# Performance work log

Measured on AMD Instinct MI355X. Metric: run time of the kernel, lower is better.

The kernel has to match this reference:

```python
import jax, jax.numpy as jnp
import numpy as np


def setup_inputs() -> dict:
    key = jax.random.key(0)
    ks = jax.random.split(key, 7)
    LAG, N, NREG, NT, H = 5, 4096, 500, 500, 16
    s = 0.05  # keep activations in a sane range
    return {
        "AX": jax.random.normal(ks[0], (LAG, N, NREG), dtype=jnp.float32),
        "W0": jax.random.normal(ks[1], (H * NT, NREG, LAG), dtype=jnp.float32) * s,
        "b0": jax.random.normal(ks[2], (H * NT,), dtype=jnp.float32) * s,
        "W1": jax.random.normal(ks[3], (NT, H, H), dtype=jnp.float32) * s,
        "b1": jax.random.normal(ks[4], (NT, H), dtype=jnp.float32) * s,
        "W2": jax.random.normal(ks[5], (NT, 1, H), dtype=jnp.float32) * s,
        "b2": jax.random.normal(ks[6], (NT, 1), dtype=jnp.float32) * s,
    }


def reference(AX, W0, b0, W1, b1, W2, b2):
    # First layer: sum_i AX[i] @ W0[:,:,lag-1-i].T + b0, fused over lag.
    # AX: [lag, N, n_regs]; W0: [hidden0*n_targets, n_regs, lag]
    x = jnp.einsum('lnr,orl->no', AX, W0[:, :, ::-1]) + b0  # [N, hidden0*nt]
    N = x.shape[0]
    nt, d1, d0 = W1.shape  # [n_targets, d_out, d_in]
    # Grouped 1x1 convs == independent per-target GEMMs; channels are target-major.
    x = x.reshape(N, nt, d0)
    x = jax.nn.relu(x)
    x = jnp.einsum('ntd,ted->nte', x, W1) + b1  # [N, nt, d1]
    x = jax.nn.relu(x)
    x = jnp.einsum('nte,tfe->ntf', x, W2) + b2  # [N, nt, 1]
    return x[..., 0]  # [N, n_targets]
```

## Files before the change

### kernel.cpp

```cpp
#include <hip/hip_runtime.h>
#include <hip/hip_bf16.h>
#include <stdint.h>

#define LAG 5
#define NROW 4096
#define NREG 500
#define NTGT 500
#define O_REAL 8000
#define KP 2560
#define NPAD 8192
#define BK 64
#define NT 40

typedef __bf16 bf16x8 __attribute__((ext_vector_type(8)));
typedef float f32x4 __attribute__((ext_vector_type(4)));

__device__ __forceinline__ unsigned short f2bf(float f) {
  unsigned u = __float_as_uint(f);
  return (unsigned short)((u + 0x7fffu + ((u >> 16) & 1u)) >> 16);
}

__device__ __forceinline__ void async16(void* lds_base, const void* g) {
  __builtin_amdgcn_global_load_lds(
      (const __attribute__((address_space(1))) unsigned int*)g,
      (__attribute__((address_space(3))) unsigned int*)lds_base,
      16, 0, 0);
}

__global__ __launch_bounds__(256) void convA(const float* __restrict__ AX,
                                             unsigned short* __restrict__ Ab) {
  int idx = blockIdx.x * 256 + threadIdx.x;
  if (idx >= NROW * (KP / 4)) return;
  int n = idx / (KP / 4);
  int c4 = idx - n * (KP / 4);
  int k = c4 * 4;
  ushort4 o;
  if (k < LAG * NREG) {
    int l = k / NREG, r = k - l * NREG;
    float4 v = *(const float4*)(AX + ((size_t)l * NROW + n) * NREG + r);
    o.x = f2bf(v.x); o.y = f2bf(v.y); o.z = f2bf(v.z); o.w = f2bf(v.w);
  } else {
    o.x = 0; o.y = 0; o.z = 0; o.w = 0;
  }
  *(ushort4*)(Ab + (size_t)idx * 4) = o;
}

__global__ __launch_bounds__(256) void convB(const float* __restrict__ W0,
                                             unsigned short* __restrict__ Bb) {
  int idx = blockIdx.x * 256 + threadIdx.x;
  if (idx >= O_REAL * NREG) return;
  int o = idx / NREG, r = idx - o * NREG;
  const float* s = W0 + (size_t)idx * LAG;
  #pragma unroll
  for (int j = 0; j < LAG; ++j)
    Bb[(size_t)o * KP + (size_t)(LAG - 1 - j) * NREG + r] = f2bf(s[j]);
}

__global__ __launch_bounds__(256) void padB(unsigned short* __restrict__ Bb) {
  int idx = blockIdx.x * 256 + threadIdx.x;
  const int A4 = O_REAL * 15;
  ushort4 z; z.x = 0; z.y = 0; z.z = 0; z.w = 0;
  if (idx < A4) {
    int row = idx / 15, c4 = idx - row * 15;
    *(ushort4*)(Bb + (size_t)row * KP + 2500 + c4 * 4) = z;
  } else {
    int j = idx - A4;
    if (j < 192 * (KP / 4))
      *(ushort4*)(Bb + (size_t)O_REAL * KP + (size_t)j * 4) = z;
  }
}

__global__ __launch_bounds__(512, 2) void gemm8(const unsigned short* __restrict__ A,
                                                const unsigned short* __restrict__ B,
                                                const float* __restrict__ b0,
                                                const float* __restrict__ W1g,
                                                const float* __restrict__ b1g,
                                                const float* __restrict__ W2g,
                                                const float* __restrict__ b2g,
                                                float* __restrict__ out) {
  extern __shared__ char smem[];
  char* sAc = smem;
  char* sBc = smem + 65536;

  int bid = blockIdx.x;
  int swz = (bid & 7) * 64 + (bid >> 3);
  int mt = swz & 15, ntile = swz >> 4;
  int row0 = mt * 256, col0 = ntile * 256;

  int tid = threadIdx.x, l = tid & 63, w = tid >> 6;
  int wr = w >> 2, wc = w & 3;

  int sr = l >> 3;
  int ss = (l & 7) ^ sr;
  const unsigned short* gApre0 = A + (size_t)(row0 + (w * 2 + 0) * 8 + sr) * KP + ss * 8;
  const unsigned short* gApre1 = A + (size_t)(row0 + (w * 2 + 1) * 8 + sr) * KP + ss * 8;
  const unsigned short* gBpre0 = B + (size_t)(col0 + (w * 2 + 0) * 8 + sr) * KP + ss * 8;
  const unsigned short* gBpre1 = B + (size_t)(col0 + (w * 2 + 1) * 8 + sr) * KP + ss * 8;

#define STG_A(buf, half, t) do { \
    async16(sAc + (buf) * 32768 + (half) * 16384 + (w * 2 + 0) * 1024, gApre0 + (size_t)(half) * 128 * KP + (size_t)(t) * BK); \
    async16(sAc + (buf) * 32768 + (half) * 16384 + (w * 2 + 1) * 1024, gApre1 + (size_t)(half) * 128 * KP + (size_t)(t) * BK); \
  } while (0)
#define STG_B(buf, half, t) do { \
    async16(sBc + (buf) * 32768 + (half) * 16384 + (w * 2 + 0) * 1024, gBpre0 + (size_t)(half) * 128 * KP + (size_t)(t) * BK); \
    async16(sBc + (buf) * 32768 + (half) * 16384 + (w * 2 + 1) * 1024, gBpre1 + (size_t)(half) * 128 * KP + (size_t)(t) * BK); \
  } while (0)

  int arowb = (wr * 128 + (l & 15)) * 128;
  int browb = (wc * 64 + (l & 15)) * 128;
  int c0 = (((l >> 4) << 4)) ^ ((l & 7) << 4);

  auto lda = [&](int buf, int mi, int kk) -> bf16x8 {
    return *(const bf16x8*)(sAc + buf * 32768 + arowb + mi * 2048 + (c0 ^ (kk * 64)));
  };
  auto ldb = [&](int buf, int ni, int kk) -> bf16x8 {
    return *(const bf16x8*)(sBc + buf * 32768 + browb + ni * 2048 + (c0 ^ (kk * 64)));
  };

  f32x4 acc[8][4];
  #pragma unroll
  for (int i = 0; i < 8; ++i)
    #pragma unroll
    for (int j = 0; j < 4; ++j) acc[i][j] = (f32x4){0.f, 0.f, 0.f, 0.f};

#define PH_SYNC() do { __builtin_amdgcn_s_barrier(); \
    asm volatile("s_waitcnt lgkmcnt(0)" ::: "memory"); \
    __builtin_amdgcn_s_setprio(1); } while (0)
#define PH_END() do { __builtin_amdgcn_s_setprio(0); __builtin_amdgcn_s_barrier(); } while (0)

#define MFMA_Q(MOFF, AF, NIOFF) do { \
    _Pragma("unroll") \
    for (int mi = 0; mi < 4; ++mi) { \
      _Pragma("unroll") \
      for (int ni = 0; ni < 2; ++ni) { \
        acc[(MOFF) + mi][(NIOFF) + ni] = __builtin_amdgcn_mfma_f32_16x16x32_bf16(AF[mi][0], bb[(NIOFF) + ni][0], acc[(MOFF) + mi][(NIOFF) + ni], 0, 0, 0); \
        acc[(MOFF) + mi][(NIOFF) + ni] = __builtin_amdgcn_mfma_f32_16x16x32_bf16(AF[mi][1], bb[(NIOFF) + ni][1], acc[(MOFF) + mi][(NIOFF) + ni], 0, 0, 0); \
      } \
    } \
  } while (0)

  STG_B(0, 0, 0); STG_B(0, 1, 0); STG_A(0, 0, 0); STG_A(0, 1, 0);
  STG_B(1, 0, 1); STG_B(1, 1, 1);
  asm volatile("s_waitcnt vmcnt(4)" ::: "memory");
  __builtin_amdgcn_s_barrier();

  for (int t = 0; t < NT; t += 2) {
    const bool last = (t == NT - 2);
    bf16x8 a03[4][2], a47[4][2], bb[4][2];

    #pragma unroll
    for (int ni = 0; ni < 2; ++ni) { bb[ni][0] = ldb(0, ni, 0); bb[ni][1] = ldb(0, ni, 1); }
    #pragma unroll
    for (int mi = 0; mi < 4; ++mi) { a03[mi][0] = lda(0, mi, 0); a03[mi][1] = lda(0, mi, 1); }
    STG_A(1, 0, t + 1);
    asm volatile("s_waitcnt lgkmcnt(8)" ::: "memory");
    PH_SYNC(); MFMA_Q(0, a03, 0); PH_END();

    #pragma unroll
    for (int ni = 2; ni < 4; ++ni) { bb[ni][0] = ldb(0, ni, 0); bb[ni][1] = ldb(0, ni, 1); }
    STG_A(1, 1, t + 1);
    PH_SYNC(); MFMA_Q(0, a03, 2); PH_END();

    #pragma unroll
    for (int mi = 0; mi < 4; ++mi) { a47[mi][0] = lda(0, 4 + mi, 0); a47[mi][1] = lda(0, 4 + mi, 1); }
    if (!last) STG_B(0, 0, t + 2);
    PH_SYNC(); MFMA_Q(4, a47, 0); PH_END();

    if (!last) STG_B(0, 1, t + 2);
    if (last) asm volatile("s_waitcnt vmcnt(0)" ::: "memory");
    else      asm volatile("s_waitcnt vmcnt(4)" ::: "memory");
    __builtin_amdgcn_s_barrier();
    asm volatile("s_waitcnt lgkmcnt(0)" ::: "memory");
    __builtin_amdgcn_s_setprio(1);
    MFMA_Q(4, a47, 2);
    PH_END();

    #pragma unroll
    for (int ni = 0; ni < 2; ++ni) { bb[ni][0] = ldb(1, ni, 0); bb[ni][1] = ldb(1, ni, 1); }
    #pragma unroll
    for (int mi = 0; mi < 4; ++mi) { a03[mi][0] = lda(1, mi, 0); a03[mi][1] = lda(1, mi, 1); }
    if (!last) STG_A(0, 0, t + 2);
    asm volatile("s_waitcnt lgkmcnt(8)" ::: "memory");
    PH_SYNC(); MFMA_Q(0, a03, 0); PH_END();

    #pragma unroll
    for (int ni = 2; ni < 4; ++ni) { bb[ni][0] = ldb(1, ni, 0); bb[ni][1] = ldb(1, ni, 1); }
    if (!last) STG_A(0, 1, t + 2);
    PH_SYNC(); MFMA_Q(0, a03, 2); PH_END();

    #pragma unroll
    for (int mi = 0; mi < 4; ++mi) { a47[mi][0] = lda(1, 4 + mi, 0); a47[mi][1] = lda(1, 4 + mi, 1); }
    if (!last) STG_B(1, 0, t + 3);
    PH_SYNC(); MFMA_Q(4, a47, 0); PH_END();

    if (!last) STG_B(1, 1, t + 3);
    if (last) asm volatile("s_waitcnt vmcnt(0)" ::: "memory");
    else      asm volatile("s_waitcnt vmcnt(4)" ::: "memory");
    __builtin_amdgcn_s_barrier();
    asm volatile("s_waitcnt lgkmcnt(0)" ::: "memory");
    __builtin_amdgcn_s_setprio(1);
    MFMA_Q(4, a47, 2);
    __builtin_amdgcn_s_setprio(0);
    __builtin_amdgcn_s_barrier();
  }

  int lq = l >> 4, lr = l & 15;
  int t0 = col0 >> 4;

  float bias[4];
  #pragma unroll
  for (int ni = 0; ni < 4; ++ni) {
    int gcol = col0 + wc * 64 + ni * 16 + lr;
    bias[ni] = (gcol < O_REAL) ? b0[gcol] : 0.f;
  }

  #pragma unroll
  for (int mi = 0; mi < 8; ++mi) {
    #pragma unroll
    for (int ni = 0; ni < 4; ++ni) {
      #pragma unroll
      for (int r = 0; r < 4; ++r) {
        int rowL = wr * 128 + mi * 16 + lq * 4 + r;
        int colL = wc * 64 + ni * 16 + lr;
        int sw = ((rowL ^ (rowL >> 2)) & 7) << 4;
        float v = fmaxf(acc[mi][ni][r] + bias[ni], 0.f);
        *(unsigned short*)(smem + (size_t)rowL * 512 + ((colL * 2) ^ sw)) = f2bf(v);
      }
    }
  }
  __syncthreads();

  int uw = __builtin_amdgcn_readfirstlane(w);
  float oacc[2][4];
  #pragma unroll
  for (int g = 0; g < 2; ++g) {
    int tloc = uw * 2 + g;
    int tt = t0 + tloc;
    bool tvalid = (tt < NTGT);
    const float* w1t = W1g + (size_t)tt * 256;
    float b1v[16], w2v[16];
    float b2v = 0.f;
    if (tvalid) {
      #pragma unroll
      for (int e4 = 0; e4 < 4; ++e4) {
        float4 ba = *(const float4*)(b1g + (size_t)tt * 16 + e4 * 4);
        float4 wa = *(const float4*)(W2g + (size_t)tt * 16 + e4 * 4);
        b1v[e4 * 4 + 0] = ba.x; b1v[e4 * 4 + 1] = ba.y; b1v[e4 * 4 + 2] = ba.z; b1v[e4 * 4 + 3] = ba.w;
        w2v[e4 * 4 + 0] = wa.x; w2v[e4 * 4 + 1] = wa.y; w2v[e4 * 4 + 2] = wa.z; w2v[e4 * 4 + 3] = wa.w;
      }
      b2v = b2g[tt];
    }
    #pragma unroll
    for (int rg = 0; rg < 4; ++rg) {
      int rowL = rg * 64 + l;
      int sw = ((rowL ^ (rowL >> 2)) & 7) << 4;
      const char* bp = smem + (size_t)rowL * 512;
      uint4 va = *(const uint4*)(bp + ((tloc * 32) ^ sw));
      uint4 vb = *(const uint4*)(bp + ((tloc * 32 + 16) ^ sw));
      unsigned q0 = va.x, q1 = va.y, q2 = va.z, q3 = va.w;
      unsigned q4 = vb.x, q5 = vb.y, q6 = vb.z, q7 = vb.w;
      float x[16];
      x[0]  = __uint_as_float(q0 << 16); x[1]  = __uint_as_float(q0 & 0xffff0000u);
      x[2]  = __uint_as_float(q1 << 16); x[3]  = __uint_as_float(q1 & 0xffff0000u);
      x[4]  = __uint_as_float(q2 << 16); x[5]  = __uint_as_float(q2 & 0xffff0000u);
      x[6]  = __uint_as_float(q3 << 16); x[7]  = __uint_as_float(q3 & 0xffff0000u);
      x[8]  = __uint_as_float(q4 << 16); x[9]  = __uint_as_float(q4 & 0xffff0000u);
      x[10] = __uint_as_float(q5 << 16); x[11] = __uint_as_float(q5 & 0xffff0000u);
      x[12] = __uint_as_float(q6 << 16); x[13] = __uint_as_float(q6 & 0xffff0000u);
      x[14] = __uint_as_float(q7 << 16); x[15] = __uint_as_float(q7 & 0xffff0000u);
      float o = 0.f;
      if (tvalid) {
        #pragma unroll
        for (int e = 0; e < 16; ++e) {
          float4 wq0 = *(const float4*)(w1t + e * 16 + 0);
          float4 wq1 = *(const float4*)(w1t + e * 16 + 4);
          float4 wq2 = *(const float4*)(w1t + e * 16 + 8);
          float4 wq3 = *(const float4*)(w1t + e * 16 + 12);
          float s = b1v[e];
          s = fmaf(x[0],  wq0.x, s); s = fmaf(x[1],  wq0.y, s);
          s = fmaf(x[2],  wq0.z, s); s = fmaf(x[3],  wq0.w, s);
          s = fmaf(x[4],  wq1.x, s); s = fmaf(x[5],  wq1.y, s);
          s = fmaf(x[6],  wq1.z, s); s = fmaf(x[7],  wq1.w, s);
          s = fmaf(x[8],  wq2.x, s); s = fmaf(x[9],  wq2.y, s);
          s = fmaf(x[10], wq2.z, s); s = fmaf(x[11], wq2.w, s);
          s = fmaf(x[12], wq3.x, s); s = fmaf(x[13], wq3.y, s);
          s = fmaf(x[14], wq3.z, s); s = fmaf(x[15], wq3.w, s);
          s = fmaxf(s, 0.f);
          o = fmaf(s, w2v[e], o);
        }
        o += b2v;
      }
      oacc[g][rg] = o;
    }
  }
  __syncthreads();

  {
    float* sOut = (float*)smem;
    #pragma unroll
    for (int g = 0; g < 2; ++g) {
      int tloc = uw * 2 + g;
      #pragma unroll
      for (int rg = 0; rg < 4; ++rg)
        sOut[(rg * 64 + l) * 17 + tloc] = oacc[g][rg];
    }
    __syncthreads();
    int c = tid & 15, rr = tid >> 4;
    bool cv = (t0 + c < NTGT);
    #pragma unroll
    for (int j = 0; j < 8; ++j) {
      int row = rr + 32 * j;
      if (cv) out[(size_t)(row0 + row) * NTGT + (t0 + c)] = sOut[row * 17 + c];
    }
  }
#undef STG_A
#undef STG_B
#undef PH_SYNC
#undef PH_END
#undef MFMA_Q
}

extern "C" void kernel_launch(void* const* d_in, const int* in_sizes, int n_in,
                              void* d_out, int out_size, void* d_ws, size_t ws_size,
                              hipStream_t stream) {
  const float* AX = (const float*)d_in[0];
  const float* W0 = (const float*)d_in[1];
  const float* b0 = (const float*)d_in[2];
  const float* W1 = (const float*)d_in[3];
  const float* b1 = (const float*)d_in[4];
  const float* W2 = (const float*)d_in[5];
  const float* b2 = (const float*)d_in[6];
  float* out = (float*)d_out;

  char* ws = (char*)d_ws;
  const size_t szA = (size_t)NROW * KP * 2;
  unsigned short* Ab = (unsigned short*)ws;
  unsigned short* Bb = (unsigned short*)(ws + szA);

  hipFuncSetAttribute((const void*)gemm8, hipFuncAttributeMaxDynamicSharedMemorySize, 131072);

  convA<<<(NROW * (KP / 4) + 255) / 256, 256, 0, stream>>>(AX, Ab);
  convB<<<(O_REAL * NREG + 255) / 256, 256, 0, stream>>>(W0, Bb);
  {
    int npad4 = O_REAL * 15 + 192 * (KP / 4);
    padB<<<(npad4 + 255) / 256, 256, 0, stream>>>(Bb);
  }
  gemm8<<<(NROW / 256) * (NPAD / 256), 512, 131072, stream>>>(Ab, Bb, b0, W1, b1, W2, b2, out);
}
```

Baseline: 207.6 us.

## Switch GEMM inner loop from 16x16x32 to 32x32x16 bf16 MFMA tiles

Replaces the 16x16x32 bf16 MFMA tiling with 32x32x16 MFMA instructions. Each wave now holds 4x2 f32x16 accumulators instead of 8x4 f32x4, and the LDS fragment addressing, swizzle and epilogue row/column mapping are rewritten to match the 32x32 output layout. The aim is fewer MFMA issues and fewer LDS fragment reads per K-step, since the larger instruction reuses each operand more. The risk is a different LDS bank-conflict pattern from the new swizzle and higher register pressure from the larger fragment arrays.

```diff
diff --git a/kernel.cpp b/kernel.cpp
--- a/kernel.cpp
+++ b/kernel.cpp
@@ -14,6 +14,7 @@
 
 typedef __bf16 bf16x8 __attribute__((ext_vector_type(8)));
 typedef float f32x4 __attribute__((ext_vector_type(4)));
+typedef float f32x16 __attribute__((ext_vector_type(16)));
 
 __device__ __forceinline__ unsigned short f2bf(float f) {
   unsigned u = __float_as_uint(f);
@@ -106,36 +107,36 @@
     async16(sBc + (buf) * 32768 + (half) * 16384 + (w * 2 + 1) * 1024, gBpre1 + (size_t)(half) * 128 * KP + (size_t)(t) * BK); \
   } while (0)
 
-  int arowb = (wr * 128 + (l & 15)) * 128;
-  int browb = (wc * 64 + (l & 15)) * 128;
-  int c0 = (((l >> 4) << 4)) ^ ((l & 7) << 4);
-
-  auto lda = [&](int buf, int mi, int kk) -> bf16x8 {
-    return *(const bf16x8*)(sAc + buf * 32768 + arowb + mi * 2048 + (c0 ^ (kk * 64)));
+  int hi = l >> 5;
+  int sw8 = (l & 7) << 4;
+  int arowb = (wr * 128 + (l & 31)) * 128;
+  int browb = (wc * 64 + (l & 31)) * 128;
+
+  auto lda32 = [&](int buf, int mi, int ks) -> bf16x8 {
+    return *(const bf16x8*)(sAc + buf * 32768 + arowb + mi * 4096 + ((((ks * 2 + hi) << 4)) ^ sw8));
   };
-  auto ldb = [&](int buf, int ni, int kk) -> bf16x8 {
-    return *(const bf16x8*)(sBc + buf * 32768 + browb + ni * 2048 + (c0 ^ (kk * 64)));
+  auto ldb32 = [&](int buf, int ni, int ks) -> bf16x8 {
+    return *(const bf16x8*)(sBc + buf * 32768 + browb + ni * 4096 + ((((ks * 2 + hi) << 4)) ^ sw8));
   };
 
-  f32x4 acc[8][4];
-  #pragma unroll
-  for (int i = 0; i < 8; ++i)
-    #pragma unroll
-    for (int j = 0; j < 4; ++j) acc[i][j] = (f32x4){0.f, 0.f, 0.f, 0.f};
+  f32x16 acc[4][2];
+  #pragma unroll
+  for (int i = 0; i < 4; ++i)
+    #pragma unroll
+    for (int j = 0; j < 2; ++j)
+      #pragma unroll
+      for (int r = 0; r < 16; ++r) acc[i][j][r] = 0.f;
 
 #define PH_SYNC() do { __builtin_amdgcn_s_barrier(); \
     asm volatile("s_waitcnt lgkmcnt(0)" ::: "memory"); \
     __builtin_amdgcn_s_setprio(1); } while (0)
 #define PH_END() do { __builtin_amdgcn_s_setprio(0); __builtin_amdgcn_s_barrier(); } while (0)
 
-#define MFMA_Q(MOFF, AF, NIOFF) do { \
+#define MFMA_P(M0, AF, BV, NI) do { \
     _Pragma("unroll") \
-    for (int mi = 0; mi < 4; ++mi) { \
-      _Pragma("unroll") \
-      for (int ni = 0; ni < 2; ++ni) { \
-        acc[(MOFF) + mi][(NIOFF) + ni] = __builtin_amdgcn_mfma_f32_16x16x32_bf16(AF[mi][0], bb[(NIOFF) + ni][0], acc[(MOFF) + mi][(NIOFF) + ni], 0, 0, 0); \
-        acc[(MOFF) + mi][(NIOFF) + ni] = __builtin_amdgcn_mfma_f32_16x16x32_bf16(AF[mi][1], bb[(NIOFF) + ni][1], acc[(MOFF) + mi][(NIOFF) + ni], 0, 0, 0); \
-      } \
+    for (int ks = 0; ks < 4; ++ks) { \
+      acc[(M0) + 0][NI] = __builtin_amdgcn_mfma_f32_32x32x16_bf16(AF[0][ks], BV[ks], acc[(M0) + 0][NI], 0, 0, 0); \
+      acc[(M0) + 1][NI] = __builtin_amdgcn_mfma_f32_32x32x16_bf16(AF[1][ks], BV[ks], acc[(M0) + 1][NI], 0, 0, 0); \
     } \
   } while (0)
 
@@ -146,25 +147,29 @@
 
   for (int t = 0; t < NT; t += 2) {
     const bool last = (t == NT - 2);
-    bf16x8 a03[4][2], a47[4][2], bb[4][2];
-
-    #pragma unroll
-    for (int ni = 0; ni < 2; ++ni) { bb[ni][0] = ldb(0, ni, 0); bb[ni][1] = ldb(0, ni, 1); }
-    #pragma unroll
-    for (int mi = 0; mi < 4; ++mi) { a03[mi][0] = lda(0, mi, 0); a03[mi][1] = lda(0, mi, 1); }
+    bf16x8 a01[2][4], a23[2][4], b0v[4], b1v[4];
+
+    #pragma unroll
+    for (int ks = 0; ks < 4; ++ks) b0v[ks] = ldb32(0, 0, ks);
+    #pragma unroll
+    for (int mi = 0; mi < 2; ++mi)
+      #pragma unroll
+      for (int ks = 0; ks < 4; ++ks) a01[mi][ks] = lda32(0, mi, ks);
     STG_A(1, 0, t + 1);
     asm volatile("s_waitcnt lgkmcnt(8)" ::: "memory");
-    PH_SYNC(); MFMA_Q(0, a03, 0); PH_END();
-
-    #pragma unroll
-    for (int ni = 2; ni < 4; ++ni) { bb[ni][0] = ldb(0, ni, 0); bb[ni][1] = ldb(0, ni, 1); }
+    PH_SYNC(); MFMA_P(0, a01, b0v, 0); PH_END();
+
+    #pragma unroll
+    for (int ks = 0; ks < 4; ++ks) b1v[ks] = ldb32(0, 1, ks);
     STG_A(1, 1, t + 1);
-    PH_SYNC(); MFMA_Q(0, a03, 2); PH_END();
-
-    #pragma unroll
-    for (int mi = 0; mi < 4; ++mi) { a47[mi][0] = lda(0, 4 + mi, 0); a47[mi][1] = lda(0, 4 + mi, 1); }
+    PH_SYNC(); MFMA_P(0, a01, b1v, 1); PH_END();
+
+    #pragma unroll
+    for (int mi = 0; mi < 2; ++mi)
+      #pragma unroll
+      for (int ks = 0; ks < 4; ++ks) a23[mi][ks] = lda32(0, 2 + mi, ks);
     if (!last) STG_B(0, 0, t + 2);
-    PH_SYNC(); MFMA_Q(4, a47, 0); PH_END();
+    PH_SYNC(); MFMA_P(2, a23, b0v, 0); PH_END();
 
     if (!last) STG_B(0, 1, t + 2);
     if (last) asm volatile("s_waitcnt vmcnt(0)" ::: "memory");
@@ -172,26 +177,30 @@
     __builtin_amdgcn_s_barrier();
     asm volatile("s_waitcnt lgkmcnt(0)" ::: "memory");
     __builtin_amdgcn_s_setprio(1);
-    MFMA_Q(4, a47, 2);
+    MFMA_P(2, a23, b1v, 1);
     PH_END();
 
     #pragma unroll
-    for (int ni = 0; ni < 2; ++ni) { bb[ni][0] = ldb(1, ni, 0); bb[ni][1] = ldb(1, ni, 1); }
-    #pragma unroll
-    for (int mi = 0; mi < 4; ++mi) { a03[mi][0] = lda(1, mi, 0); a03[mi][1] = lda(1, mi, 1); }
+    for (int ks = 0; ks < 4; ++ks) b0v[ks] = ldb32(1, 0, ks);
+    #pragma unroll
+    for (int mi = 0; mi < 2; ++mi)
+      #pragma unroll
+      for (int ks = 0; ks < 4; ++ks) a01[mi][ks] = lda32(1, mi, ks);
     if (!last) STG_A(0, 0, t + 2);
     asm volatile("s_waitcnt lgkmcnt(8)" ::: "memory");
-    PH_SYNC(); MFMA_Q(0, a03, 0); PH_END();
-
-    #pragma unroll
-    for (int ni = 2; ni < 4; ++ni) { bb[ni][0] = ldb(1, ni, 0); bb[ni][1] = ldb(1, ni, 1); }
+    PH_SYNC(); MFMA_P(0, a01, b0v, 0); PH_END();
+
+    #pragma unroll
+    for (int ks = 0; ks < 4; ++ks) b1v[ks] = ldb32(1, 1, ks);
     if (!last) STG_A(0, 1, t + 2);
-    PH_SYNC(); MFMA_Q(0, a03, 2); PH_END();
-
-    #pragma unroll
-    for (int mi = 0; mi < 4; ++mi) { a47[mi][0] = lda(1, 4 + mi, 0); a47[mi][1] = lda(1, 4 + mi, 1); }
+    PH_SYNC(); MFMA_P(0, a01, b1v, 1); PH_END();
+
+    #pragma unroll
+    for (int mi = 0; mi < 2; ++mi)
+      #pragma unroll
+      for (int ks = 0; ks < 4; ++ks) a23[mi][ks] = lda32(1, 2 + mi, ks);
     if (!last) STG_B(1, 0, t + 3);
-    PH_SYNC(); MFMA_Q(4, a47, 0); PH_END();
+    PH_SYNC(); MFMA_P(2, a23, b0v, 0); PH_END();
 
     if (!last) STG_B(1, 1, t + 3);
     if (last) asm volatile("s_waitcnt vmcnt(0)" ::: "memory");
@@ -199,31 +208,30 @@
     __builtin_amdgcn_s_barrier();
     asm volatile("s_waitcnt lgkmcnt(0)" ::: "memory");
     __builtin_amdgcn_s_setprio(1);
-    MFMA_Q(4, a47, 2);
+    MFMA_P(2, a23, b1v, 1);
     __builtin_amdgcn_s_setprio(0);
     __builtin_amdgcn_s_barrier();
   }
 
-  int lq = l >> 4, lr = l & 15;
   int t0 = col0 >> 4;
 
-  float bias[4];
-  #pragma unroll
-  for (int ni = 0; ni < 4; ++ni) {
-    int gcol = col0 + wc * 64 + ni * 16 + lr;
-    bias[ni] = (gcol < O_REAL) ? b0[gcol] : 0.f;
-  }
-
-  #pragma unroll
-  for (int mi = 0; mi < 8; ++mi) {
-    #pragma unroll
-    for (int ni = 0; ni < 4; ++ni) {
-      #pragma unroll
-      for (int r = 0; r < 4; ++r) {
-        int rowL = wr * 128 + mi * 16 + lq * 4 + r;
-        int colL = wc * 64 + ni * 16 + lr;
+  float bias2[2];
+  #pragma unroll
+  for (int ni = 0; ni < 2; ++ni) {
+    int gcol = col0 + wc * 64 + ni * 32 + (l & 31);
+    bias2[ni] = (gcol < O_REAL) ? b0[gcol] : 0.f;
+  }
+
+  #pragma unroll
+  for (int mi = 0; mi < 4; ++mi) {
+    #pragma unroll
+    for (int ni = 0; ni < 2; ++ni) {
+      #pragma unroll
+      for (int reg = 0; reg < 16; ++reg) {
+        int rowL = wr * 128 + mi * 32 + (reg & 3) + 8 * (reg >> 2) + 4 * (l >> 5);
+        int colL = wc * 64 + ni * 32 + (l & 31);
         int sw = ((rowL ^ (rowL >> 2)) & 7) << 4;
-        float v = fmaxf(acc[mi][ni][r] + bias[ni], 0.f);
+        float v = fmaxf(acc[mi][ni][reg] + bias2[ni], 0.f);
         *(unsigned short*)(smem + (size_t)rowL * 512 + ((colL * 2) ^ sw)) = f2bf(v);
       }
     }
@@ -238,14 +246,14 @@
     int tt = t0 + tloc;
     bool tvalid = (tt < NTGT);
     const float* w1t = W1g + (size_t)tt * 256;
-    float b1v[16], w2v[16];
+    float b1v2[16], w2v[16];
     float b2v = 0.f;
     if (tvalid) {
       #pragma unroll
       for (int e4 = 0; e4 < 4; ++e4) {
         float4 ba = *(const float4*)(b1g + (size_t)tt * 16 + e4 * 4);
         float4 wa = *(const float4*)(W2g + (size_t)tt * 16 + e4 * 4);
-        b1v[e4 * 4 + 0] = ba.x; b1v[e4 * 4 + 1] = ba.y; b1v[e4 * 4 + 2] = ba.z; b1v[e4 * 4 + 3] = ba.w;
+        b1v2[e4 * 4 + 0] = ba.x; b1v2[e4 * 4 + 1] = ba.y; b1v2[e4 * 4 + 2] = ba.z; b1v2[e4 * 4 + 3] = ba.w;
         w2v[e4 * 4 + 0] = wa.x; w2v[e4 * 4 + 1] = wa.y; w2v[e4 * 4 + 2] = wa.z; w2v[e4 * 4 + 3] = wa.w;
       }
       b2v = b2g[tt];
@@ -276,7 +284,7 @@
           float4 wq1 = *(const float4*)(w1t + e * 16 + 4);
           float4 wq2 = *(const float4*)(w1t + e * 16 + 8);
           float4 wq3 = *(const float4*)(w1t + e * 16 + 12);
-          float s = b1v[e];
+          float s = b1v2[e];
           s = fmaf(x[0],  wq0.x, s); s = fmaf(x[1],  wq0.y, s);
           s = fmaf(x[2],  wq0.z, s); s = fmaf(x[3],  wq0.w, s);
           s = fmaf(x[4],  wq1.x, s); s = fmaf(x[5],  wq1.y, s);
@@ -317,7 +325,7 @@
 #undef STG_B
 #undef PH_SYNC
 #undef PH_END
-#undef MFMA_Q
+#undef MFMA_P
 }
 
 extern "C" void kernel_launch(void* const* d_in, const int* in_sizes, int n_in,
```

After: 223.8 us. 1.08x slower.
